# Optimization experiments

Measured on AMD Instinct MI355X. Metric: run time of the kernel, lower is better.

Reference implementation:

```python
import jax, jax.numpy as jnp
import numpy as np


def _conv2d(x, w, pad):
    # x: (B,Cin,H,W), w: (Cout,Cin,kh,kw), NCHW conv
    return jax.lax.conv_general_dilated(
        x, w, window_strides=(1, 1), padding=[(pad, pad), (pad, pad)],
        dimension_numbers=('NCHW', 'OIHW', 'NCHW'))


def _bilinear_upsample_ac(x, s):
    # F.interpolate(mode='bilinear', align_corners=True), x: (B,C,H,W) -> (B,C,H*s,W*s)
    B, C, H, W = x.shape
    Hs, Ws = H * s, W * s

    def idx_w(n_out, n_in):
        pos = jnp.arange(n_out, dtype=x.dtype) * ((n_in - 1) / (n_out - 1))
        i0 = jnp.floor(pos).astype(jnp.int32)
        i1 = jnp.minimum(i0 + 1, n_in - 1)
        return i0, i1, (pos - i0).astype(x.dtype)

    y0, y1, wy = idx_w(Hs, H)
    x0, x1, wx = idx_w(Ws, W)
    t = x[:, :, y0, :] * (1 - wy)[None, None, :, None] + x[:, :, y1, :] * wy[None, None, :, None]
    return t[:, :, :, x0] * (1 - wx) + t[:, :, :, x1] * wx


def _grid_sample_border_ac(img, grid):
    # F.grid_sample(mode='bilinear', padding_mode='border', align_corners=True)
    # img: (N,C,H,W), grid: (N,Ho,Wo,2) with (x,y) in [-1,1]
    N, C, H, W = img.shape
    ix = jnp.clip((grid[..., 0] + 1) * 0.5 * (W - 1), 0.0, W - 1)
    iy = jnp.clip((grid[..., 1] + 1) * 0.5 * (H - 1), 0.0, H - 1)
    x0 = jnp.floor(ix).astype(jnp.int32); x1 = jnp.minimum(x0 + 1, W - 1)
    y0 = jnp.floor(iy).astype(jnp.int32); y1 = jnp.minimum(y0 + 1, H - 1)
    wx = (ix - x0)[..., None]
    wy = (iy - y0)[..., None]
    imgh = jnp.transpose(img, (0, 2, 3, 1))  # (N,H,W,C)
    b = jnp.arange(N)[:, None, None]
    v00 = imgh[b, y0, x0]; v01 = imgh[b, y0, x1]
    v10 = imgh[b, y1, x0]; v11 = imgh[b, y1, x1]
    out = (v00 * (1 - wx) + v01 * wx) * (1 - wy) + (v10 * (1 - wx) + v11 * wx) * wy
    return jnp.transpose(out, (0, 3, 1, 2))


def setup_inputs() -> dict:
    key = jax.random.key(0)
    ks = jax.random.split(key, 4)
    B, C, H, W, G = 16, 128, 64, 64, 4
    return {
        'x': jax.random.normal(ks[0], (B, C, H, W), jnp.float32),
        'w_off': jax.random.normal(ks[1], (2 * G, C, 3, 3), jnp.float32) * 0.02,
        'b_off': jnp.zeros((2 * G,), jnp.float32),
        'w_proj': jax.random.normal(ks[2], (C, C, 1, 1), jnp.float32) * 0.05,
        'bn_gamma': jnp.ones((C,), jnp.float32),
        'bn_beta': jnp.zeros((C,), jnp.float32),
        'bn_mean': jnp.zeros((C,), jnp.float32),
        'bn_var': jnp.ones((C,), jnp.float32),
        'scale': 2,
        'groups': 4,
    }


def reference(x, w_off, b_off, w_proj, bn_gamma, bn_beta, bn_mean, bn_var, scale, groups):
    B, C, H, W = x.shape
    s, G = scale, groups
    Hs, Ws = H * s, W * s
    Cg = C // G
    eps = 1e-5

    # offset branch: 3x3 conv + bias, tanh
    off = jnp.tanh(_conv2d(x, w_off, 1) + b_off[None, :, None, None])  # (B,2G,H,W)

    # proj branch: 1x1 conv (no bias) + BN(eval) + SiLU
    p = _conv2d(x, w_proj, 0)
    p = (p - bn_mean[None, :, None, None]) * (bn_gamma / jnp.sqrt(bn_var + eps))[None, :, None, None] \
        + bn_beta[None, :, None, None]
    p = p * jax.nn.sigmoid(p)

    # base sampling grid (x,y) in [-1,1]
    yy, xx = jnp.meshgrid(jnp.linspace(-1.0, 1.0, Hs, dtype=x.dtype),
                          jnp.linspace(-1.0, 1.0, Ws, dtype=x.dtype), indexing='ij')
    base = jnp.stack([xx, yy], axis=-1)  # (Hs,Ws,2)

    # upsample offsets for all groups at once, add scaled to base
    o_up = _bilinear_upsample_ac(off, s)                     # (B,2G,Hs,Ws)
    o_up = o_up.reshape(B, G, 2, Hs, Ws).transpose(0, 1, 3, 4, 2)  # (B,G,Hs,Ws,2)
    grid = base[None, None] + o_up * (2.0 / max(Hs, Ws))     # (B,G,Hs,Ws,2)

    # fold groups into batch and grid_sample once
    xg = p.reshape(B * G, Cg, H, W)
    out = _grid_sample_border_ac(xg, grid.reshape(B * G, Hs, Ws, 2))
    return out.reshape(B, C, Hs, Ws)
```

## Files before the change

### kernel.cpp

```cpp
#include <hip/hip_runtime.h>
#include <math.h>

#define BN_ 16
#define C_ 128
#define H_ 64
#define W_ 64
#define G_ 4
#define HS_ 128
#define WS_ 128
#define CG_ 32
#define HW_ (H_*W_)
#define HWS_ (HS_*WS_)
#define NOFF_ (BN_*8*HW_)

__global__ void prep_w(const float* __restrict__ w_proj, const float* __restrict__ g,
                       const float* __restrict__ be, const float* __restrict__ mean,
                       const float* __restrict__ var, float* __restrict__ wT,
                       float* __restrict__ b2) {
    int i = blockIdx.x * 256 + threadIdx.x;
    if (i < C_ * C_) {
        int k = i >> 7, co = i & 127;
        float a = g[co] / sqrtf(var[co] + 1e-5f);
        wT[i] = w_proj[co * C_ + k] * a;
    } else if (i < C_ * C_ + C_) {
        int co = i - C_ * C_;
        float a = g[co] / sqrtf(var[co] + 1e-5f);
        b2[co] = be[co] - mean[co] * a;
    }
}

__global__ __launch_bounds__(256) void conv_off(const float* __restrict__ x,
                                                const float* __restrict__ w_off,
                                                float* __restrict__ part) {
    int bx = blockIdx.x;
    int cc = bx & 7;
    int rt = (bx >> 3) & 7;
    int b  = bx >> 6;
    int t  = threadIdx.x;
    int row = t >> 5;
    int cb  = (t & 31) * 2;

    __shared__ float xs[8][10][66];
    __shared__ float wsh[8][9][8];

    float acc[8][2];
#pragma unroll
    for (int i = 0; i < 8; ++i) { acc[i][0] = 0.f; acc[i][1] = 0.f; }

    int row0 = rt * 8;
    int ch_s = (t >> 4) & 7;
    int q_s  = t & 15;
    int rbase = (t >> 7) * 5;

    for (int sub = 0; sub < 2; ++sub) {
        int cbase = cc * 16 + sub * 8;
        __syncthreads();
#pragma unroll
        for (int it = 0; it < 5; ++it) {
            int r = rbase + it;
            int grow = row0 + r - 1;
            float4 v = make_float4(0.f, 0.f, 0.f, 0.f);
            if (grow >= 0 && grow < H_)
                v = *(const float4*)&x[((size_t)(b * C_ + cbase + ch_s) * H_ + grow) * W_ + q_s * 4];
            xs[ch_s][r][1 + q_s * 4] = v.x;
            xs[ch_s][r][2 + q_s * 4] = v.y;
            xs[ch_s][r][3 + q_s * 4] = v.z;
            xs[ch_s][r][4 + q_s * 4] = v.w;
        }
        if (t < 128) {
            int ch2 = t >> 4, r2 = t & 15;
            if (r2 < 10) { xs[ch2][r2][0] = 0.f; xs[ch2][r2][65] = 0.f; }
        }
        for (int i = t; i < 576; i += 256) {
            int co  = i & 7;
            int tap = (i >> 3) % 9;
            int ch3 = (i >> 3) / 9;
            wsh[ch3][tap][co] = w_off[(co * C_ + cbase + ch3) * 9 + tap];
        }
        __syncthreads();
#pragma unroll
        for (int ch = 0; ch < 8; ++ch) {
#pragma unroll
            for (int ky = 0; ky < 3; ++ky) {
                float2 xv01 = *(float2*)&xs[ch][row + ky][cb];
                float2 xv23 = *(float2*)&xs[ch][row + ky][cb + 2];
                float xa[4] = {xv01.x, xv01.y, xv23.x, xv23.y};
#pragma unroll
                for (int kx = 0; kx < 3; ++kx) {
                    float4 w0 = *(float4*)&wsh[ch][ky * 3 + kx][0];
                    float4 w1 = *(float4*)&wsh[ch][ky * 3 + kx][4];
                    float wv[8] = {w0.x, w0.y, w0.z, w0.w, w1.x, w1.y, w1.z, w1.w};
                    float x0 = xa[kx], x1 = xa[kx + 1];
#pragma unroll
                    for (int co = 0; co < 8; ++co) {
                        acc[co][0] += x0 * wv[co];
                        acc[co][1] += x1 * wv[co];
                    }
                }
            }
        }
    }
#pragma unroll
    for (int co = 0; co < 8; ++co) {
        float2 v = make_float2(acc[co][0], acc[co][1]);
        *(float2*)&part[((size_t)(cc * BN_ + b) * 8 + co) * HW_ + (row0 + row) * W_ + cb] = v;
    }
}

__global__ void off_reduce(const float* __restrict__ part, const float* __restrict__ b_off,
                           float* __restrict__ off) {
    int i = (blockIdx.x * 256 + threadIdx.x) * 4;
    if (i >= NOFF_) return;
    float4 s = *(const float4*)&part[i];
#pragma unroll
    for (int j = 1; j < 8; ++j) {
        float4 a = *(const float4*)&part[(size_t)j * NOFF_ + i];
        s.x += a.x; s.y += a.y; s.z += a.z; s.w += a.w;
    }
    int co = (i / HW_) & 7;
    float bb = b_off[co];
    float4 r;
    r.x = tanhf(s.x + bb);
    r.y = tanhf(s.y + bb);
    r.z = tanhf(s.z + bb);
    r.w = tanhf(s.w + bb);
    *(float4*)&off[i] = r;
}

__global__ __launch_bounds__(256) void conv_proj(const float* __restrict__ x,
                                                 const float* __restrict__ wT,
                                                 const float* __restrict__ b2,
                                                 float* __restrict__ p) {
    int bx = blockIdx.x;
    int b = bx >> 5;
    int pos0 = (bx & 31) * 128;
    int t = threadIdx.x;
    int cob = (t >> 4) * 8;
    int pb0 = (t & 15) * 4;

    __shared__ float xs[16][128];
    __shared__ float wsh[16][128];

    float acc[8][8];
#pragma unroll
    for (int i = 0; i < 8; ++i)
#pragma unroll
        for (int j = 0; j < 8; ++j) acc[i][j] = 0.f;

    for (int k0 = 0; k0 < C_; k0 += 16) {
        __syncthreads();
#pragma unroll
        for (int j = 0; j < 2; ++j) {
            int idx = j * 1024 + t * 4;
            int k = idx >> 7, pp = idx & 127;
            *(float4*)&xs[k][pp]  = *(const float4*)&x[(size_t)(b * C_ + k0 + k) * HW_ + pos0 + pp];
            *(float4*)&wsh[k][pp] = *(const float4*)&wT[(k0 + k) * C_ + pp];
        }
        __syncthreads();
#pragma unroll
        for (int k = 0; k < 16; ++k) {
            float4 xv0 = *(float4*)&xs[k][pb0];
            float4 xv1 = *(float4*)&xs[k][pb0 + 64];
            float4 w0  = *(float4*)&wsh[k][cob];
            float4 w1  = *(float4*)&wsh[k][cob + 4];
            float xa[8] = {xv0.x, xv0.y, xv0.z, xv0.w, xv1.x, xv1.y, xv1.z, xv1.w};
            float wa[8] = {w0.x, w0.y, w0.z, w0.w, w1.x, w1.y, w1.z, w1.w};
#pragma unroll
            for (int co = 0; co < 8; ++co)
#pragma unroll
                for (int j = 0; j < 8; ++j)
                    acc[co][j] += wa[co] * xa[j];
        }
    }
#pragma unroll
    for (int co = 0; co < 8; ++co) {
        float bb = b2[cob + co];
        float v[8];
#pragma unroll
        for (int j = 0; j < 8; ++j) {
            float a = acc[co][j] + bb;
            v[j] = a / (1.f + __expf(-a));
        }
        float* dst = &p[(size_t)(b * C_ + cob + co) * HW_ + pos0];
        *(float4*)&dst[pb0]      = make_float4(v[0], v[1], v[2], v[3]);
        *(float4*)&dst[pb0 + 64] = make_float4(v[4], v[5], v[6], v[7]);
    }
}

__global__ __launch_bounds__(256) void dysample(const float* __restrict__ p,
                                                const float* __restrict__ off,
                                                float* __restrict__ out) {
    int bx = blockIdx.x;
    int t  = threadIdx.x;
    int ys = (bx & 63) * 2 + (t >> 7);
    int g  = (bx >> 6) & 3;
    int b  = bx >> 8;
    int xsid = t & 127;

    const float rw = 63.0f / 127.0f;
    float py = ys * rw;
    int uy0 = (int)floorf(py);
    float fy = py - (float)uy0;
    int uy1 = min(uy0 + 1, 63);
    float pxf = xsid * rw;
    int ux0 = (int)floorf(pxf);
    float fx = pxf - (float)ux0;
    int ux1 = min(ux0 + 1, 63);

    const float* o0 = off + (size_t)(b * 8 + 2 * g) * HW_;
    const float* o1 = o0 + HW_;
    float ox, oy;
    {
        float a00 = o0[uy0 * 64 + ux0], a01 = o0[uy0 * 64 + ux1];
        float a10 = o0[uy1 * 64 + ux0], a11 = o0[uy1 * 64 + ux1];
        float t0 = a00 * (1.f - fy) + a10 * fy;
        float t1 = a01 * (1.f - fy) + a11 * fy;
        ox = t0 * (1.f - fx) + t1 * fx;
    }
    {
        float a00 = o1[uy0 * 64 + ux0], a01 = o1[uy0 * 64 + ux1];
        float a10 = o1[uy1 * 64 + ux0], a11 = o1[uy1 * 64 + ux1];
        float t0 = a00 * (1.f - fy) + a10 * fy;
        float t1 = a01 * (1.f - fy) + a11 * fy;
        oy = t0 * (1.f - fx) + t1 * fx;
    }

    float gx = (-1.f + xsid * (2.0f / 127.0f)) + ox * (2.0f / 128.0f);
    float gy = (-1.f + ys   * (2.0f / 127.0f)) + oy * (2.0f / 128.0f);

    float ix = fminf(fmaxf((gx + 1.f) * 0.5f * 63.f, 0.f), 63.f);
    float iy = fminf(fmaxf((gy + 1.f) * 0.5f * 63.f, 0.f), 63.f);
    int sx0 = (int)floorf(ix);
    int sx1 = min(sx0 + 1, 63);
    float wx = ix - (float)sx0;
    int sy0 = (int)floorf(iy);
    int sy1 = min(sy0 + 1, 63);
    float wy = iy - (float)sy0;

    int o00 = sy0 * 64 + sx0, o01 = sy0 * 64 + sx1;
    int o10 = sy1 * 64 + sx0, o11 = sy1 * 64 + sx1;
    const float* pbase = p + (size_t)(b * C_ + g * CG_) * HW_;
    float* obase = out + (size_t)(b * C_ + g * CG_) * HWS_ + ys * WS_ + xsid;
    float w00 = (1.f - wx) * (1.f - wy), w01 = wx * (1.f - wy);
    float w10 = (1.f - wx) * wy,         w11 = wx * wy;
#pragma unroll 4
    for (int c = 0; c < CG_; ++c) {
        const float* pc = pbase + (size_t)c * HW_;
        float r = pc[o00] * w00 + pc[o01] * w01 + pc[o10] * w10 + pc[o11] * w11;
        __builtin_nontemporal_store(r, &obase[(size_t)c * HWS_]);
    }
}

extern "C" void kernel_launch(void* const* d_in, const int* in_sizes, int n_in,
                              void* d_out, int out_size, void* d_ws, size_t ws_size,
                              hipStream_t stream) {
    const float* x      = (const float*)d_in[0];
    const float* w_off  = (const float*)d_in[1];
    const float* b_off  = (const float*)d_in[2];
    const float* w_proj = (const float*)d_in[3];
    const float* bn_g   = (const float*)d_in[4];
    const float* bn_b   = (const float*)d_in[5];
    const float* bn_m   = (const float*)d_in[6];
    const float* bn_v   = (const float*)d_in[7];
    float* out = (float*)d_out;
    float* ws  = (float*)d_ws;

    float* p    = ws;
    float* part = ws;
    float* offb = ws + 8388608;
    float* wT   = ws + 8912896;
    float* b2   = ws + 8929280;

    prep_w    <<<65,   256, 0, stream>>>(w_proj, bn_g, bn_b, bn_m, bn_v, wT, b2);
    conv_off  <<<1024, 256, 0, stream>>>(x, w_off, part);
    off_reduce<<<512,  256, 0, stream>>>(part, b_off, offb);
    conv_proj <<<512,  256, 0, stream>>>(x, wT, b2, p);
    dysample  <<<4096, 256, 0, stream>>>(p, offb, out);
}
```

Before: 265.2 us.

## Stage halo rows of projected features in LDS for grid sampling

The grid-sample kernel now loads a 3-row band (clamped halo) of each group's 32 projected channels into shared memory, then does all bilinear gathers from LDS instead of from global memory. This relies on the tanh-bounded offset keeping each sample within one source row of the block's row. Separately, the 1x1 projection conv uses a 64-position tile with 8x4 accumulators and twice as many blocks, trading register reuse for occupancy. The added LDS footprint and a barrier may limit dysample occupancy.

```diff
diff --git a/kernel.cpp b/kernel.cpp
--- a/kernel.cpp
+++ b/kernel.cpp
@@ -132,58 +132,57 @@
                                                  const float* __restrict__ b2,
                                                  float* __restrict__ p) {
     int bx = blockIdx.x;
-    int b = bx >> 5;
-    int pos0 = (bx & 31) * 128;
+    int b = bx >> 6;
+    int pos0 = (bx & 63) * 64;
     int t = threadIdx.x;
     int cob = (t >> 4) * 8;
-    int pb0 = (t & 15) * 4;
-
-    __shared__ float xs[16][128];
+    int pb  = (t & 15) * 4;
+
+    __shared__ float xs[16][64];
     __shared__ float wsh[16][128];
 
-    float acc[8][8];
+    float acc[8][4];
 #pragma unroll
     for (int i = 0; i < 8; ++i)
 #pragma unroll
-        for (int j = 0; j < 8; ++j) acc[i][j] = 0.f;
+        for (int j = 0; j < 4; ++j) acc[i][j] = 0.f;
+
+    int ks = t >> 4;
+    int ps = (t & 15) * 4;
 
     for (int k0 = 0; k0 < C_; k0 += 16) {
         __syncthreads();
-#pragma unroll
-        for (int j = 0; j < 2; ++j) {
-            int idx = j * 1024 + t * 4;
-            int k = idx >> 7, pp = idx & 127;
-            *(float4*)&xs[k][pp]  = *(const float4*)&x[(size_t)(b * C_ + k0 + k) * HW_ + pos0 + pp];
-            *(float4*)&wsh[k][pp] = *(const float4*)&wT[(k0 + k) * C_ + pp];
-        }
+        *(float4*)&xs[ks][ps] = *(const float4*)&x[(size_t)(b * C_ + k0 + ks) * HW_ + pos0 + ps];
+        int co8 = (t & 15) * 8;
+        *(float4*)&wsh[ks][co8]     = *(const float4*)&wT[(k0 + ks) * C_ + co8];
+        *(float4*)&wsh[ks][co8 + 4] = *(const float4*)&wT[(k0 + ks) * C_ + co8 + 4];
         __syncthreads();
 #pragma unroll
         for (int k = 0; k < 16; ++k) {
-            float4 xv0 = *(float4*)&xs[k][pb0];
-            float4 xv1 = *(float4*)&xs[k][pb0 + 64];
-            float4 w0  = *(float4*)&wsh[k][cob];
-            float4 w1  = *(float4*)&wsh[k][cob + 4];
-            float xa[8] = {xv0.x, xv0.y, xv0.z, xv0.w, xv1.x, xv1.y, xv1.z, xv1.w};
+            float4 xv = *(float4*)&xs[k][pb];
+            float4 w0 = *(float4*)&wsh[k][cob];
+            float4 w1 = *(float4*)&wsh[k][cob + 4];
             float wa[8] = {w0.x, w0.y, w0.z, w0.w, w1.x, w1.y, w1.z, w1.w};
 #pragma unroll
-            for (int co = 0; co < 8; ++co)
-#pragma unroll
-                for (int j = 0; j < 8; ++j)
-                    acc[co][j] += wa[co] * xa[j];
+            for (int co = 0; co < 8; ++co) {
+                acc[co][0] += wa[co] * xv.x;
+                acc[co][1] += wa[co] * xv.y;
+                acc[co][2] += wa[co] * xv.z;
+                acc[co][3] += wa[co] * xv.w;
+            }
         }
     }
 #pragma unroll
     for (int co = 0; co < 8; ++co) {
         float bb = b2[cob + co];
-        float v[8];
-#pragma unroll
-        for (int j = 0; j < 8; ++j) {
+        float v[4];
+#pragma unroll
+        for (int j = 0; j < 4; ++j) {
             float a = acc[co][j] + bb;
             v[j] = a / (1.f + __expf(-a));
         }
-        float* dst = &p[(size_t)(b * C_ + cob + co) * HW_ + pos0];
-        *(float4*)&dst[pb0]      = make_float4(v[0], v[1], v[2], v[3]);
-        *(float4*)&dst[pb0 + 64] = make_float4(v[4], v[5], v[6], v[7]);
+        *(float4*)&p[(size_t)(b * C_ + cob + co) * HW_ + pos0 + pb] =
+            make_float4(v[0], v[1], v[2], v[3]);
     }
 }
 
@@ -191,10 +190,27 @@
                                                 const float* __restrict__ off,
                                                 float* __restrict__ out) {
     int bx = blockIdx.x;
-    int t  = threadIdx.x;
-    int ys = (bx & 63) * 2 + (t >> 7);
+    int rp = bx & 63;
     int g  = (bx >> 6) & 3;
     int b  = bx >> 8;
+    int t  = threadIdx.x;
+
+    __shared__ float ls[CG_][3][64];
+
+    const float* pg = p + (size_t)(b * C_ + g * CG_) * HW_;
+#pragma unroll
+    for (int it = 0; it < 6; ++it) {
+        int f = it * 256 + t;
+        int ch = f / 48;
+        int rem = f - ch * 48;
+        int rw_ = rem >> 4;
+        int wq = (rem & 15) << 2;
+        int grow = min(max(rp - 1 + rw_, 0), 63);
+        float4 v = *(const float4*)&pg[(size_t)ch * HW_ + grow * 64 + wq];
+        *(float4*)&ls[ch][rw_][wq] = v;
+    }
+
+    int ys = rp * 2 + (t >> 7);
     int xsid = t & 127;
 
     const float rw = 63.0f / 127.0f;
@@ -234,19 +250,22 @@
     int sx1 = min(sx0 + 1, 63);
     float wx = ix - (float)sx0;
     int sy0 = (int)floorf(iy);
-    int sy1 = min(sy0 + 1, 63);
     float wy = iy - (float)sy0;
 
-    int o00 = sy0 * 64 + sx0, o01 = sy0 * 64 + sx1;
-    int o10 = sy1 * 64 + sx0, o11 = sy1 * 64 + sx1;
-    const float* pbase = p + (size_t)(b * C_ + g * CG_) * HW_;
-    float* obase = out + (size_t)(b * C_ + g * CG_) * HWS_ + ys * WS_ + xsid;
+    int ry0 = sy0 - rp + 1;
+    int ry1 = min(sy0 + 1, 63) - rp + 1;
+
     float w00 = (1.f - wx) * (1.f - wy), w01 = wx * (1.f - wy);
     float w10 = (1.f - wx) * wy,         w11 = wx * wy;
-#pragma unroll 4
+
+    __syncthreads();
+
+    float* obase = out + (size_t)(b * C_ + g * CG_) * HWS_ + ys * WS_ + xsid;
+#pragma unroll 8
     for (int c = 0; c < CG_; ++c) {
-        const float* pc = pbase + (size_t)c * HW_;
-        float r = pc[o00] * w00 + pc[o01] * w01 + pc[o10] * w10 + pc[o11] * w11;
+        float v00 = ls[c][ry0][sx0], v01 = ls[c][ry0][sx1];
+        float v10 = ls[c][ry1][sx0], v11 = ls[c][ry1][sx1];
+        float r = v00 * w00 + v01 * w01 + v10 * w10 + v11 * w11;
         __builtin_nontemporal_store(r, &obase[(size_t)c * HWS_]);
     }
 }
@@ -274,6 +293,6 @@
     prep_w    <<<65,   256, 0, stream>>>(w_proj, bn_g, bn_b, bn_m, bn_v, wT, b2);
     conv_off  <<<1024, 256, 0, stream>>>(x, w_off, part);
     off_reduce<<<512,  256, 0, stream>>>(part, b_off, offb);
-    conv_proj <<<512,  256, 0, stream>>>(x, wT, b2, p);
+    conv_proj <<<1024, 256, 0, stream>>>(x, wT, b2, p);
     dysample  <<<4096, 256, 0, stream>>>(p, offb, out);
 }
```

Result: faster. 244.1 us (-8.0%).
